# Kernel tuning notes

Measured on AMD Instinct MI355X. Metric: run time of the kernel, lower is better.

Reference implementation:

```python
import jax, jax.numpy as jnp
import numpy as np


def _graph_conv(x, W, b, src, dst, norm_src, norm_dst, n_nodes):
    # DGL GraphConv, norm='both': out = D_in^{-1/2} * A * D_out^{-1/2} * x * W + b
    h = x * norm_src[:, None]                      # [N, d] scale by src out-degree norm
    m = h[src]                                     # [E, d] gather (irregular access)
    agg = jax.ops.segment_sum(m, dst, num_segments=n_nodes)  # [N, d] scatter-add
    agg = agg * norm_dst[:, None]
    return agg @ W + b


def setup_inputs() -> dict:
    key = jax.random.key(0)
    ks = jax.random.split(key, 6)
    N, E, IN, HID = 50000, 800000, 64, 128
    in_feat = jax.random.normal(ks[0], (N, IN), dtype=jnp.float32)
    W1 = jax.random.normal(ks[1], (IN, HID), dtype=jnp.float32) * (1.0 / np.sqrt(IN))
    b1 = jnp.zeros((HID,), dtype=jnp.float32)
    W2 = jax.random.normal(ks[2], (HID, IN), dtype=jnp.float32) * (1.0 / np.sqrt(HID))
    b2 = jnp.zeros((IN,), dtype=jnp.float32)
    src = jax.random.randint(ks[3], (E,), 0, N, dtype=jnp.int32)
    dst = jax.random.randint(ks[4], (E,), 0, N, dtype=jnp.int32)
    return {"in_feat": in_feat, "W1": W1, "b1": b1, "W2": W2, "b2": b2,
            "src": src, "dst": dst, "n_nodes": N}


def reference(in_feat, W1, b1, W2, b2, src, dst, n_nodes):
    ones = jnp.ones(src.shape, dtype=in_feat.dtype)
    deg_out = jax.ops.segment_sum(ones, src, num_segments=n_nodes)
    deg_in = jax.ops.segment_sum(ones, dst, num_segments=n_nodes)
    # DGL clamps degrees to min 1 (allow_zero_in_degree=True just skips the check)
    norm_src = jnp.clip(deg_out, 1.0, None) ** -0.5
    norm_dst = jnp.clip(deg_in, 1.0, None) ** -0.5
    h = _graph_conv(in_feat, W1, b1, src, dst, norm_src, norm_dst, n_nodes)
    h = jax.nn.relu(h)
    h = _graph_conv(h, W2, b2, src, dst, norm_src, norm_dst, n_nodes)
    return h
```

## Files before the change

kernel.cpp:

```cpp
#include <hip/hip_runtime.h>

#define IN_F 64
#define HID_F 128
#define CAP 64
#define CHUNK 4096
#define CAPB 4096
#define MAXB 512

typedef unsigned short u16;
typedef unsigned int u32;
typedef _Float16 f16;
typedef __attribute__((ext_vector_type(4))) _Float16 f16x4;
typedef __attribute__((ext_vector_type(8))) _Float16 f16x8;
typedef __attribute__((ext_vector_type(4))) float f32x4;

__global__ __launch_bounds__(256)
void partition_kernel(const int* __restrict__ src, const int* __restrict__ dst,
                      int* __restrict__ gcurD, int* __restrict__ gcurS,
                      u32* __restrict__ bufD, u16* __restrict__ bufS,
                      const float* __restrict__ W1, const float* __restrict__ W2,
                      f16* __restrict__ W1t, f16* __restrict__ W2t,
                      int E, int NBUCK) {
    if (blockIdx.x == gridDim.x - 1) {
        for (int t = threadIdx.x; t < 2 * IN_F * HID_F; t += 256) {
            if (t < IN_F * HID_F) {
                int n = t / IN_F, k = t % IN_F;
                W1t[t] = (f16)W1[k * HID_F + n];
            } else {
                int i = t - IN_F * HID_F;
                int n = i / HID_F, k = i % HID_F;
                W2t[i] = (f16)W2[k * IN_F + n];
            }
        }
        return;
    }
    __shared__ int histD[MAXB], histS[MAXB], baseD[MAXB], baseS[MAXB];
    const int t  = threadIdx.x;
    const int e0 = blockIdx.x * CHUNK;
    const int n  = min(CHUNK, E - e0);

    for (int b = t; b < NBUCK; b += 256) { histD[b] = 0; histS[b] = 0; }
    __syncthreads();
    for (int i = t; i < n; i += 256) {
        atomicAdd(&histD[dst[e0 + i] >> 7], 1);
        atomicAdd(&histS[src[e0 + i] >> 7], 1);
    }
    __syncthreads();
    for (int b = t; b < NBUCK; b += 256) {
        baseD[b] = atomicAdd(&gcurD[b], histD[b]);
        baseS[b] = atomicAdd(&gcurS[b], histS[b]);
        histD[b] = 0;
        histS[b] = 0;
    }
    __syncthreads();
    for (int i = t; i < n; i += 256) {
        int d  = dst[e0 + i];
        int s  = src[e0 + i];
        int bD = d >> 7, bS = s >> 7;
        int p  = baseD[bD] + atomicAdd(&histD[bD], 1);
        if (p < CAPB) bufD[(size_t)bD * CAPB + p] = (u32)d | ((u32)s << 16);
        int p2 = baseS[bS] + atomicAdd(&histS[bS], 1);
        if (p2 < CAPB) bufS[(size_t)bS * CAPB + p2] = (u16)s;
    }
}

__global__ __launch_bounds__(256)
void bucket_pass2_kernel(const u32* __restrict__ bufD, const int* __restrict__ gcurD,
                         const u16* __restrict__ bufS, const int* __restrict__ gcurS,
                         u16* __restrict__ slots, int* __restrict__ deg_in,
                         float* __restrict__ norm_dst, float* __restrict__ norm_src,
                         const float* __restrict__ x, f16x4* __restrict__ scaled_x,
                         int N, int NBUCK) {
    __shared__ int lcur[128];
    const int t = threadIdx.x;
    if (t < 128) lcur[t] = 0;
    __syncthreads();
    if (blockIdx.x < NBUCK) {
        const int b = blockIdx.x;
        const int cnt = min(gcurD[b], CAPB);
        const u32* p = bufD + (size_t)b * CAPB;
        for (int i = t; i < cnt; i += 256) {
            u32 v = p[i];
            int d = (int)(v & 0xFFFFu);
            int s = (int)(v >> 16);
            int pos = atomicAdd(&lcur[d & 127], 1);
            if (pos < CAP) slots[(size_t)d * CAP + pos] = (u16)s;
        }
        __syncthreads();
        int node = b * 128 + t;
        if (t < 128 && node < N) {
            deg_in[node]   = lcur[t];
            norm_dst[node] = rsqrtf((float)max(lcur[t], 1));
        }
    } else {
        const int b = blockIdx.x - NBUCK;
        const int cnt = min(gcurS[b], CAPB);
        const u16* p = bufS + (size_t)b * CAPB;
        for (int i = t; i < cnt; i += 256)
            atomicAdd(&lcur[p[i] & 127], 1);
        __syncthreads();
        int node0 = b * 128;
        if (t < 128 && node0 + t < N)
            norm_src[node0 + t] = rsqrtf((float)max(lcur[t], 1));
        for (int i = t; i < 128 * 16; i += 256) {
            int r = i >> 4, c = i & 15;
            int node = node0 + r;
            if (node < N) {
                float ns = rsqrtf((float)max(lcur[r], 1));
                float4 v = ((const float4*)x)[(size_t)node * 16 + c];
                f16x4 h;
                h.x = (f16)(v.x * ns); h.y = (f16)(v.y * ns);
                h.z = (f16)(v.z * ns); h.w = (f16)(v.w * ns);
                scaled_x[(size_t)node * 16 + c] = h;
            }
        }
    }
}

__global__ __launch_bounds__(256)
void gather_gemm_kernel(const f16x4* __restrict__ x, const u16* __restrict__ slots,
                        const int* __restrict__ deg_in,
                        const f16* __restrict__ W1t, const float* __restrict__ b1,
                        const float* __restrict__ nd, const float* __restrict__ ns,
                        const f16* __restrict__ W2t, f16* __restrict__ g2, int N) {
    constexpr int LDX = IN_F + 8;
    constexpr int LDH = HID_F + 8;
    __shared__ __align__(16) f16 sx[16 * LDX];
    __shared__ __align__(16) f16 h[16 * LDH];

    const int t   = threadIdx.x;
    const int row = t >> 4;
    const int c   = t & 15;
    const int r0  = blockIdx.x * 16;
    const int node = r0 + row;

    float4 acc = make_float4(0.f, 0.f, 0.f, 0.f);
    if (node < N) {
        int deg = min(deg_in[node], CAP);
        const u16* srow = slots + (size_t)node * CAP;
        int i = 0;
        for (; i + 8 <= deg; i += 8) {
            int s[8];
#pragma unroll
            for (int j = 0; j < 8; ++j) s[j] = (int)srow[i + j];
            f16x4 v[8];
#pragma unroll
            for (int j = 0; j < 8; ++j) v[j] = x[(size_t)s[j] * 16 + c];
#pragma unroll
            for (int j = 0; j < 8; ++j) {
                acc.x += (float)v[j].x; acc.y += (float)v[j].y;
                acc.z += (float)v[j].z; acc.w += (float)v[j].w;
            }
        }
        for (; i < deg; ++i) {
            f16x4 v = x[(size_t)srow[i] * 16 + c];
            acc.x += (float)v.x; acc.y += (float)v.y;
            acc.z += (float)v.z; acc.w += (float)v.w;
        }
    }
    {
        f16x4 hv;
        hv.x = (f16)acc.x; hv.y = (f16)acc.y; hv.z = (f16)acc.z; hv.w = (f16)acc.w;
        *(f16x4*)&sx[row * LDX + c * 4] = hv;
    }
    __syncthreads();

    const int wave = t >> 6;
    const int lane = t & 63;
    const int nl   = lane & 15;
    const int quad = lane >> 4;

    f16x8 a1[2];
#pragma unroll
    for (int kf = 0; kf < 2; ++kf)
        a1[kf] = *(const f16x8*)(sx + nl * LDX + kf * 32 + quad * 8);

    float rs1[4];
#pragma unroll
    for (int reg = 0; reg < 4; ++reg)
        rs1[reg] = nd[min(r0 + quad * 4 + reg, N - 1)];

#pragma unroll
    for (int cti = 0; cti < 2; ++cti) {
        const int ct = wave * 2 + cti;
        f32x4 acc1 = (f32x4){0.f, 0.f, 0.f, 0.f};
#pragma unroll
        for (int kf = 0; kf < 2; ++kf) {
            f16x8 b = *(const f16x8*)(W1t + (ct * 16 + nl) * IN_F + kf * 32 + quad * 8);
            acc1 = __builtin_amdgcn_mfma_f32_16x16x32_f16(a1[kf], b, acc1, 0, 0, 0);
        }
        float bb = b1[ct * 16 + nl];
#pragma unroll
        for (int reg = 0; reg < 4; ++reg) {
            float v = fmaxf(acc1[reg] * rs1[reg] + bb, 0.f);
            h[(quad * 4 + reg) * LDH + ct * 16 + nl] = (f16)v;
        }
    }
    __syncthreads();

    f32x4 acc2 = (f32x4){0.f, 0.f, 0.f, 0.f};
#pragma unroll
    for (int kf = 0; kf < 4; ++kf) {
        f16x8 a2 = *(const f16x8*)(h + nl * LDH + kf * 32 + quad * 8);
        f16x8 b  = *(const f16x8*)(W2t + (wave * 16 + nl) * HID_F + kf * 32 + quad * 8);
        acc2 = __builtin_amdgcn_mfma_f32_16x16x32_f16(a2, b, acc2, 0, 0, 0);
    }

    float rs2[4];
#pragma unroll
    for (int reg = 0; reg < 4; ++reg)
        rs2[reg] = ns[min(r0 + quad * 4 + reg, N - 1)];
#pragma unroll
    for (int reg = 0; reg < 4; ++reg) {
        int r = r0 + quad * 4 + reg;
        if (r < N)
            g2[(size_t)r * IN_F + wave * 16 + nl] = (f16)(acc2[reg] * rs2[reg]);
    }
}

__global__ void gather_out_kernel(const f16x4* __restrict__ x, const u16* __restrict__ slots,
                                  const int* __restrict__ deg_in, const float* __restrict__ sd,
                                  const float* __restrict__ bias,
                                  float4* __restrict__ out, int N) {
    int t = blockIdx.x * blockDim.x + threadIdx.x;
    int node = t >> 4;
    int c = t & 15;
    if (node >= N) return;
    int deg = min(deg_in[node], CAP);
    const u16* srow = slots + (size_t)node * CAP;
    float4 acc = make_float4(0.f, 0.f, 0.f, 0.f);

    int i = 0;
    for (; i + 8 <= deg; i += 8) {
        int s[8];
#pragma unroll
        for (int j = 0; j < 8; ++j) s[j] = (int)srow[i + j];
        f16x4 v[8];
#pragma unroll
        for (int j = 0; j < 8; ++j) v[j] = x[(size_t)s[j] * 16 + c];
#pragma unroll
        for (int j = 0; j < 8; ++j) {
            acc.x += (float)v[j].x; acc.y += (float)v[j].y;
            acc.z += (float)v[j].z; acc.w += (float)v[j].w;
        }
    }
    for (; i < deg; ++i) {
        f16x4 v = x[(size_t)srow[i] * 16 + c];
        acc.x += (float)v.x; acc.y += (float)v.y;
        acc.z += (float)v.z; acc.w += (float)v.w;
    }
    float d = sd[node];
    float4 bb = ((const float4*)bias)[c];
    acc.x = acc.x * d + bb.x;
    acc.y = acc.y * d + bb.y;
    acc.z = acc.z * d + bb.z;
    acc.w = acc.w * d + bb.w;
    out[t] = acc;
}

extern "C" void kernel_launch(void* const* d_in, const int* in_sizes, int n_in,
                              void* d_out, int out_size, void* d_ws, size_t ws_size,
                              hipStream_t stream) {
    const float* in_feat = (const float*)d_in[0];
    const float* W1      = (const float*)d_in[1];
    const float* b1      = (const float*)d_in[2];
    const float* W2      = (const float*)d_in[3];
    const float* b2      = (const float*)d_in[4];
    const int*   src     = (const int*)d_in[5];
    const int*   dst     = (const int*)d_in[6];

    const int N = in_sizes[0] / IN_F;
    const int E = in_sizes[5];
    float* out = (float*)d_out;

    const int NBUCK = (N + 127) >> 7;

    int* deg_in  = (int*)d_ws;
    int* gcurD   = deg_in + N;
    int* gcurS   = gcurD + MAXB;
    u16* slots   = (u16*)(gcurS + MAXB);
    float* norm_src = (float*)(slots + (size_t)N * CAP);
    float* norm_dst = norm_src + N;
    f16* scaled_x = (f16*)(norm_dst + N);
    f16* g2       = scaled_x + (size_t)N * IN_F;
    f16* W1t      = g2 + (size_t)N * IN_F;
    f16* W2t      = W1t + IN_F * HID_F;
    u32* bufD     = (u32*)(W2t + IN_F * HID_F);
    u16* bufS     = (u16*)(bufD + (size_t)NBUCK * CAPB);

    hipMemsetAsync(gcurD, 0, sizeof(int) * 2 * MAXB, stream);
    partition_kernel<<<(E + CHUNK - 1) / CHUNK + 1, 256, 0, stream>>>(
        src, dst, gcurD, gcurS, bufD, bufS, W1, W2, W1t, W2t, E, NBUCK);

    bucket_pass2_kernel<<<2 * NBUCK, 256, 0, stream>>>(
        bufD, gcurD, bufS, gcurS, slots, deg_in, norm_dst, norm_src,
        in_feat, (f16x4*)scaled_x, N, NBUCK);

    gather_gemm_kernel<<<(N + 15) / 16, 256, 0, stream>>>(
        (const f16x4*)scaled_x, slots, deg_in, W1t, b1, norm_dst, norm_src,
        W2t, g2, N);

    gather_out_kernel<<<(N * 16 + 255) / 256, 256, 0, stream>>>(
        (const f16x4*)g2, slots, deg_in, norm_dst, b2, (float4*)out, N);
}
```

Baseline: 169.4 us.

## Widen gathers to 16-byte f16x8 loads and cache edge ids in partition

The gather loops in both aggregation kernels now use 8 threads per node with 16-byte f16x8 loads instead of 16 threads with 8-byte loads. The gather-GEMM block therefore covers 32 nodes and runs two MFMA row tiles. The partition kernel keeps each thread's 16 src/dst values in registers between the histogram and scatter passes, so edge arrays are read once instead of twice. The aim is fewer, wider memory transactions and less redundant global traffic, at the cost of more registers per thread and fewer threads in flight for latency hiding.

```diff
diff --git a/kernel.cpp b/kernel.cpp
--- a/kernel.cpp
+++ b/kernel.cpp
@@ -39,11 +39,19 @@
     const int e0 = blockIdx.x * CHUNK;
     const int n  = min(CHUNK, E - e0);
 
+    int ed[16], es[16];
+
     for (int b = t; b < NBUCK; b += 256) { histD[b] = 0; histS[b] = 0; }
     __syncthreads();
-    for (int i = t; i < n; i += 256) {
-        atomicAdd(&histD[dst[e0 + i] >> 7], 1);
-        atomicAdd(&histS[src[e0 + i] >> 7], 1);
+#pragma unroll
+    for (int j = 0; j < 16; ++j) {
+        int i = t + j * 256;
+        if (i < n) {
+            ed[j] = dst[e0 + i];
+            es[j] = src[e0 + i];
+            atomicAdd(&histD[ed[j] >> 7], 1);
+            atomicAdd(&histS[es[j] >> 7], 1);
+        }
     }
     __syncthreads();
     for (int b = t; b < NBUCK; b += 256) {
@@ -53,14 +61,18 @@
         histS[b] = 0;
     }
     __syncthreads();
-    for (int i = t; i < n; i += 256) {
-        int d  = dst[e0 + i];
-        int s  = src[e0 + i];
-        int bD = d >> 7, bS = s >> 7;
-        int p  = baseD[bD] + atomicAdd(&histD[bD], 1);
-        if (p < CAPB) bufD[(size_t)bD * CAPB + p] = (u32)d | ((u32)s << 16);
-        int p2 = baseS[bS] + atomicAdd(&histS[bS], 1);
-        if (p2 < CAPB) bufS[(size_t)bS * CAPB + p2] = (u16)s;
+#pragma unroll
+    for (int j = 0; j < 16; ++j) {
+        int i = t + j * 256;
+        if (i < n) {
+            int d  = ed[j];
+            int s  = es[j];
+            int bD = d >> 7, bS = s >> 7;
+            int p  = baseD[bD] + atomicAdd(&histD[bD], 1);
+            if (p < CAPB) bufD[(size_t)bD * CAPB + p] = (u32)d | ((u32)s << 16);
+            int p2 = baseS[bS] + atomicAdd(&histS[bS], 1);
+            if (p2 < CAPB) bufS[(size_t)bS * CAPB + p2] = (u16)s;
+        }
     }
 }
 
@@ -118,23 +130,25 @@
 }
 
 __global__ __launch_bounds__(256)
-void gather_gemm_kernel(const f16x4* __restrict__ x, const u16* __restrict__ slots,
+void gather_gemm_kernel(const f16x8* __restrict__ xs, const u16* __restrict__ slots,
                         const int* __restrict__ deg_in,
                         const f16* __restrict__ W1t, const float* __restrict__ b1,
                         const float* __restrict__ nd, const float* __restrict__ ns,
                         const f16* __restrict__ W2t, f16* __restrict__ g2, int N) {
     constexpr int LDX = IN_F + 8;
     constexpr int LDH = HID_F + 8;
-    __shared__ __align__(16) f16 sx[16 * LDX];
-    __shared__ __align__(16) f16 h[16 * LDH];
+    __shared__ __align__(16) f16 sx[32 * LDX];
+    __shared__ __align__(16) f16 h[2][16 * LDH];
 
     const int t   = threadIdx.x;
-    const int row = t >> 4;
-    const int c   = t & 15;
-    const int r0  = blockIdx.x * 16;
+    const int row = t >> 3;
+    const int c   = t & 7;
+    const int r0  = blockIdx.x * 32;
     const int node = r0 + row;
 
-    float4 acc = make_float4(0.f, 0.f, 0.f, 0.f);
+    float acc[8];
+#pragma unroll
+    for (int k = 0; k < 8; ++k) acc[k] = 0.f;
     if (node < N) {
         int deg = min(deg_in[node], CAP);
         const u16* srow = slots + (size_t)node * CAP;
@@ -143,25 +157,25 @@
             int s[8];
 #pragma unroll
             for (int j = 0; j < 8; ++j) s[j] = (int)srow[i + j];
-            f16x4 v[8];
-#pragma unroll
-            for (int j = 0; j < 8; ++j) v[j] = x[(size_t)s[j] * 16 + c];
-#pragma unroll
-            for (int j = 0; j < 8; ++j) {
-                acc.x += (float)v[j].x; acc.y += (float)v[j].y;
-                acc.z += (float)v[j].z; acc.w += (float)v[j].w;
-            }
+            f16x8 v[8];
+#pragma unroll
+            for (int j = 0; j < 8; ++j) v[j] = xs[(size_t)s[j] * 8 + c];
+#pragma unroll
+            for (int j = 0; j < 8; ++j)
+#pragma unroll
+                for (int k = 0; k < 8; ++k) acc[k] += (float)v[j][k];
         }
         for (; i < deg; ++i) {
-            f16x4 v = x[(size_t)srow[i] * 16 + c];
-            acc.x += (float)v.x; acc.y += (float)v.y;
-            acc.z += (float)v.z; acc.w += (float)v.w;
+            f16x8 v = xs[(size_t)srow[i] * 8 + c];
+#pragma unroll
+            for (int k = 0; k < 8; ++k) acc[k] += (float)v[k];
         }
     }
     {
-        f16x4 hv;
-        hv.x = (f16)acc.x; hv.y = (f16)acc.y; hv.z = (f16)acc.z; hv.w = (f16)acc.w;
-        *(f16x4*)&sx[row * LDX + c * 4] = hv;
+        f16x8 hv;
+#pragma unroll
+        for (int k = 0; k < 8; ++k) hv[k] = (f16)acc[k];
+        *(f16x8*)&sx[row * LDX + c * 8] = hv;
     }
     __syncthreads();
 
@@ -170,92 +184,104 @@
     const int nl   = lane & 15;
     const int quad = lane >> 4;
 
-    f16x8 a1[2];
-#pragma unroll
-    for (int kf = 0; kf < 2; ++kf)
-        a1[kf] = *(const f16x8*)(sx + nl * LDX + kf * 32 + quad * 8);
-
-    float rs1[4];
-#pragma unroll
-    for (int reg = 0; reg < 4; ++reg)
-        rs1[reg] = nd[min(r0 + quad * 4 + reg, N - 1)];
-
-#pragma unroll
-    for (int cti = 0; cti < 2; ++cti) {
-        const int ct = wave * 2 + cti;
-        f32x4 acc1 = (f32x4){0.f, 0.f, 0.f, 0.f};
-#pragma unroll
-        for (int kf = 0; kf < 2; ++kf) {
-            f16x8 b = *(const f16x8*)(W1t + (ct * 16 + nl) * IN_F + kf * 32 + quad * 8);
-            acc1 = __builtin_amdgcn_mfma_f32_16x16x32_f16(a1[kf], b, acc1, 0, 0, 0);
-        }
-        float bb = b1[ct * 16 + nl];
+#pragma unroll
+    for (int rt = 0; rt < 2; ++rt) {
+        f16x8 a1[2];
+#pragma unroll
+        for (int kf = 0; kf < 2; ++kf)
+            a1[kf] = *(const f16x8*)(sx + (rt * 16 + nl) * LDX + kf * 32 + quad * 8);
+
+        float rs1[4];
+#pragma unroll
+        for (int reg = 0; reg < 4; ++reg)
+            rs1[reg] = nd[min(r0 + rt * 16 + quad * 4 + reg, N - 1)];
+
+        f16* hb = h[rt];
+#pragma unroll
+        for (int cti = 0; cti < 2; ++cti) {
+            const int ct = wave * 2 + cti;
+            f32x4 acc1 = (f32x4){0.f, 0.f, 0.f, 0.f};
+#pragma unroll
+            for (int kf = 0; kf < 2; ++kf) {
+                f16x8 b = *(const f16x8*)(W1t + (ct * 16 + nl) * IN_F + kf * 32 + quad * 8);
+                acc1 = __builtin_amdgcn_mfma_f32_16x16x32_f16(a1[kf], b, acc1, 0, 0, 0);
+            }
+            float bb = b1[ct * 16 + nl];
+#pragma unroll
+            for (int reg = 0; reg < 4; ++reg) {
+                float v = fmaxf(acc1[reg] * rs1[reg] + bb, 0.f);
+                hb[(quad * 4 + reg) * LDH + ct * 16 + nl] = (f16)v;
+            }
+        }
+    }
+    __syncthreads();
+
+#pragma unroll
+    for (int rt = 0; rt < 2; ++rt) {
+        f32x4 acc2 = (f32x4){0.f, 0.f, 0.f, 0.f};
+#pragma unroll
+        for (int kf = 0; kf < 4; ++kf) {
+            f16x8 a2 = *(const f16x8*)(h[rt] + nl * LDH + kf * 32 + quad * 8);
+            f16x8 b  = *(const f16x8*)(W2t + (wave * 16 + nl) * HID_F + kf * 32 + quad * 8);
+            acc2 = __builtin_amdgcn_mfma_f32_16x16x32_f16(a2, b, acc2, 0, 0, 0);
+        }
+
+        float rs2[4];
+#pragma unroll
+        for (int reg = 0; reg < 4; ++reg)
+            rs2[reg] = ns[min(r0 + rt * 16 + quad * 4 + reg, N - 1)];
 #pragma unroll
         for (int reg = 0; reg < 4; ++reg) {
-            float v = fmaxf(acc1[reg] * rs1[reg] + bb, 0.f);
-            h[(quad * 4 + reg) * LDH + ct * 16 + nl] = (f16)v;
-        }
-    }
-    __syncthreads();
-
-    f32x4 acc2 = (f32x4){0.f, 0.f, 0.f, 0.f};
-#pragma unroll
-    for (int kf = 0; kf < 4; ++kf) {
-        f16x8 a2 = *(const f16x8*)(h + nl * LDH + kf * 32 + quad * 8);
-        f16x8 b  = *(const f16x8*)(W2t + (wave * 16 + nl) * HID_F + kf * 32 + quad * 8);
-        acc2 = __builtin_amdgcn_mfma_f32_16x16x32_f16(a2, b, acc2, 0, 0, 0);
-    }
-
-    float rs2[4];
-#pragma unroll
-    for (int reg = 0; reg < 4; ++reg)
-        rs2[reg] = ns[min(r0 + quad * 4 + reg, N - 1)];
-#pragma unroll
-    for (int reg = 0; reg < 4; ++reg) {
-        int r = r0 + quad * 4 + reg;
-        if (r < N)
-            g2[(size_t)r * IN_F + wave * 16 + nl] = (f16)(acc2[reg] * rs2[reg]);
-    }
-}
-
-__global__ void gather_out_kernel(const f16x4* __restrict__ x, const u16* __restrict__ slots,
-                                  const int* __restrict__ deg_in, const float* __restrict__ sd,
-                                  const float* __restrict__ bias,
-                                  float4* __restrict__ out, int N) {
-    int t = blockIdx.x * blockDim.x + threadIdx.x;
-    int node = t >> 4;
-    int c = t & 15;
+            int r = r0 + rt * 16 + quad * 4 + reg;
+            if (r < N)
+                g2[(size_t)r * IN_F + wave * 16 + nl] = (f16)(acc2[reg] * rs2[reg]);
+        }
+    }
+}
+
+__global__ __launch_bounds__(256)
+void gather_out_kernel(const f16x8* __restrict__ xs, const u16* __restrict__ slots,
+                       const int* __restrict__ deg_in, const float* __restrict__ sd,
+                       const float* __restrict__ bias,
+                       float4* __restrict__ out, int N) {
+    int tg = blockIdx.x * blockDim.x + threadIdx.x;
+    int node = tg >> 3;
+    int c = tg & 7;
     if (node >= N) return;
     int deg = min(deg_in[node], CAP);
     const u16* srow = slots + (size_t)node * CAP;
-    float4 acc = make_float4(0.f, 0.f, 0.f, 0.f);
+    float acc[8];
+#pragma unroll
+    for (int k = 0; k < 8; ++k) acc[k] = 0.f;
 
     int i = 0;
     for (; i + 8 <= deg; i += 8) {
         int s[8];
 #pragma unroll
         for (int j = 0; j < 8; ++j) s[j] = (int)srow[i + j];
-        f16x4 v[8];
-#pragma unroll
-        for (int j = 0; j < 8; ++j) v[j] = x[(size_t)s[j] * 16 + c];
-#pragma unroll
-        for (int j = 0; j < 8; ++j) {
-            acc.x += (float)v[j].x; acc.y += (float)v[j].y;
-            acc.z += (float)v[j].z; acc.w += (float)v[j].w;
-        }
+        f16x8 v[8];
+#pragma unroll
+        for (int j = 0; j < 8; ++j) v[j] = xs[(size_t)s[j] * 8 + c];
+#pragma unroll
+        for (int j = 0; j < 8; ++j)
+#pragma unroll
+            for (int k = 0; k < 8; ++k) acc[k] += (float)v[j][k];
     }
     for (; i < deg; ++i) {
-        f16x4 v = x[(size_t)srow[i] * 16 + c];
-        acc.x += (float)v.x; acc.y += (float)v.y;
-        acc.z += (float)v.z; acc.w += (float)v.w;
+        f16x8 v = xs[(size_t)srow[i] * 8 + c];
+#pragma unroll
+        for (int k = 0; k < 8; ++k) acc[k] += (float)v[k];
     }
     float d = sd[node];
-    float4 bb = ((const float4*)bias)[c];
-    acc.x = acc.x * d + bb.x;
-    acc.y = acc.y * d + bb.y;
-    acc.z = acc.z * d + bb.z;
-    acc.w = acc.w * d + bb.w;
-    out[t] = acc;
+    float4 b0 = ((const float4*)bias)[c * 2];
+    float4 b1v = ((const float4*)bias)[c * 2 + 1];
+    float4 o0, o1;
+    o0.x = acc[0] * d + b0.x;  o0.y = acc[1] * d + b0.y;
+    o0.z = acc[2] * d + b0.z;  o0.w = acc[3] * d + b0.w;
+    o1.x = acc[4] * d + b1v.x; o1.y = acc[5] * d + b1v.y;
+    o1.z = acc[6] * d + b1v.z; o1.w = acc[7] * d + b1v.w;
+    out[(size_t)node * 16 + c * 2]     = o0;
+    out[(size_t)node * 16 + c * 2 + 1] = o1;
 }
 
 extern "C" void kernel_launch(void* const* d_in, const int* in_sizes, int n_in,
@@ -296,10 +322,10 @@
         bufD, gcurD, bufS, gcurS, slots, deg_in, norm_dst, norm_src,
         in_feat, (f16x4*)scaled_x, N, NBUCK);
 
-    gather_gemm_kernel<<<(N + 15) / 16, 256, 0, stream>>>(
-        (const f16x4*)scaled_x, slots, deg_in, W1t, b1, norm_dst, norm_src,
+    gather_gemm_kernel<<<(N + 31) / 32, 256, 0, stream>>>(
+        (const f16x8*)scaled_x, slots, deg_in, W1t, b1, norm_dst, norm_src,
         W2t, g2, N);
 
-    gather_out_kernel<<<(N * 16 + 255) / 256, 256, 0, stream>>>(
-        (const f16x4*)g2, slots, deg_in, norm_dst, b2, (float4*)out, N);
-}
+    gather_out_kernel<<<(N * 8 + 255) / 256, 256, 0, stream>>>(
+        (const f16x8*)g2, slots, deg_in, norm_dst, b2, (float4*)out, N);
+}
```

Result: no change. 167.6 us (-1.1%).
